# Optimization experiments

Hardware: AMD Instinct MI355X
Metric: run time of the kernel (lower is better)

Reference implementation:

```python
import jax, jax.numpy as jnp
import numpy as np

N, E = 100000, 1600000
NODE_IN, EDGE_IN, H = 128, 16, 128


def sage_conv(x, src, dst, Wl, Wr, b, n_nodes):
    # PyG SAGEConv (aggr='mean'): out = lin_l(mean_{j->i} x_j) + lin_r(x_i), bias on lin_l
    msg_sum = jax.ops.segment_sum(x[src], dst, num_segments=n_nodes)      # [N, d]
    cnt = jax.ops.segment_sum(jnp.ones((src.shape[0],), x.dtype), dst, num_segments=n_nodes)
    mean = msg_sum / jnp.maximum(cnt, 1.0)[:, None]                        # empty neighborhoods -> 0
    return mean @ Wl + x @ Wr + b


def setup_inputs() -> dict:
    key = jax.random.key(0)
    ks = jax.random.split(key, 12)
    s = lambda d: 1.0 / np.sqrt(d)
    return {
        "x": jax.random.normal(ks[0], (N, NODE_IN), jnp.float32),
        "edge_index": jax.random.randint(ks[1], (2, E), 0, N, dtype=jnp.int64),
        "edge_attr": jax.random.normal(ks[2], (E, EDGE_IN), jnp.float32),
        "Wl1": jax.random.normal(ks[3], (NODE_IN, H), jnp.float32) * s(NODE_IN),
        "Wr1": jax.random.normal(ks[4], (NODE_IN, H), jnp.float32) * s(NODE_IN),
        "b1": jnp.zeros((H,), jnp.float32),
        "Wl2": jax.random.normal(ks[5], (H, H), jnp.float32) * s(H),
        "Wr2": jax.random.normal(ks[6], (H, H), jnp.float32) * s(H),
        "b2": jnp.zeros((H,), jnp.float32),
        "Wm1": jax.random.normal(ks[7], (2 * H + EDGE_IN, H), jnp.float32) * s(2 * H + EDGE_IN),
        "bm1": jnp.zeros((H,), jnp.float32),
        "Wm2": jax.random.normal(ks[8], (H, 1), jnp.float32) * s(H),
        "bm2": jnp.zeros((1,), jnp.float32),
    }


def reference(x, edge_index, edge_attr, Wl1, Wr1, b1, Wl2, Wr2, b2, Wm1, bm1, Wm2, bm2):
    src, dst = edge_index[0], edge_index[1]
    h = jax.nn.relu(sage_conv(x, src, dst, Wl1, Wr1, b1, N))
    h = jax.nn.relu(sage_conv(h, src, dst, Wl2, Wr2, b2, N))
    edge_feat = jnp.concatenate([h[src], h[dst], edge_attr], axis=1)  # [E, 2H+edge_in]
    out = jax.nn.relu(edge_feat @ Wm1 + bm1) @ Wm2 + bm2               # dropout is identity in eval
    return out.reshape(-1)
```

## Files before the change

### kernel.cpp

```cpp
#include <hip/hip_runtime.h>

typedef _Float16 f16;
typedef _Float16 f16x2 __attribute__((ext_vector_type(2)));
typedef _Float16 f16x8 __attribute__((ext_vector_type(8)));
typedef float f32x4 __attribute__((ext_vector_type(4)));

#define MFMA16(a,b,c) __builtin_amdgcn_mfma_f32_16x16x32_f16((a),(b),(c),0,0,0)

__global__ void k_detect(const long long* ei, int n_nodes, int* flag) {
    long long v = ei[threadIdx.x];
    int bad = (v < 0 || v >= n_nodes);
    unsigned long long m = __ballot(bad);
    if (threadIdx.x == 0) *flag = (m == 0ULL);
}

__global__ void k_idx(const void* ei, int E, const int* __restrict__ flag,
                      int* __restrict__ src, int* __restrict__ dst,
                      int* __restrict__ deg) {
    int e = blockIdx.x * 256 + threadIdx.x;
    if (e >= E) return;
    int s, d;
    if (*flag) {
        const long long* p = (const long long*)ei;
        s = (int)p[e];
        d = (int)p[(size_t)E + e];
    } else {
        const int* p = (const int*)ei;
        s = p[e];
        d = p[(size_t)E + e];
    }
    src[e] = s;
    dst[e] = d;
    atomicAdd(&deg[d], 1);
}

__device__ __forceinline__ void wfrag_body(const float* Wa, const float* Wb,
                                           f16* dst, int t) {
    int l = t & 63;
    int s = t >> 9;
    int k0 = s * 32 + (l >> 4) * 8;
    int j = ((t >> 6) & 7) * 16 + (l & 15);
    f16x8 h;
    #pragma unroll
    for (int e = 0; e < 8; e++) {
        int k = k0 + e;
        float v = (k < 128) ? Wa[k * 128 + j] : Wb[(k - 128) * 128 + j];
        h[e] = (f16)v;
    }
    *(f16x8*)(dst + (size_t)t * 8) = h;
}

__global__ void k_prep(const float* __restrict__ x,
                       const float* __restrict__ Wl1, const float* __restrict__ Wr1,
                       const float* __restrict__ Wl2, const float* __restrict__ Wr2,
                       const float* __restrict__ Wm1,
                       f16* __restrict__ xh, f16* __restrict__ w1f, f16* __restrict__ w2f,
                       f16* __restrict__ zwf, f16* __restrict__ wef, int N) {
    const int xb = (N * 16 + 255) / 256;
    int b = blockIdx.x;
    if (b < xb) {
        int i = (b * 256 + threadIdx.x) * 8;
        if (i >= N * 128) return;
        float4 a = *(const float4*)(x + i);
        float4 c = *(const float4*)(x + i + 4);
        f16x8 h;
        h[0] = (f16)a.x; h[1] = (f16)a.y; h[2] = (f16)a.z; h[3] = (f16)a.w;
        h[4] = (f16)c.x; h[5] = (f16)c.y; h[6] = (f16)c.z; h[7] = (f16)c.w;
        *(f16x8*)(xh + i) = h;
        return;
    }
    b -= xb;
    if (b < 16) {
        wfrag_body(Wl1, Wr1, w1f, b * 256 + threadIdx.x);
        return;
    }
    if (b < 32) {
        wfrag_body(Wl2, Wr2, w2f, (b - 16) * 256 + threadIdx.x);
        return;
    }
    if (b < 48) {
        int t = (b - 32) * 256 + threadIdx.x;
        int lane = t & 63, c = (t >> 6) & 15, s = t >> 10;
        int k0 = s * 32 + (lane >> 4) * 8;
        int j = c * 16 + (lane & 15);
        f16x8 h;
        #pragma unroll
        for (int e = 0; e < 8; e++) {
            int k = k0 + e;
            float v = (j < 128) ? Wm1[k * 128 + j] : Wm1[(128 + k) * 128 + (j - 128)];
            h[e] = (f16)v;
        }
        *(f16x8*)(zwf + (size_t)t * 8) = h;
        return;
    }
    {
        int t = (b - 48) * 256 + threadIdx.x;
        if (t >= 8 * 64) return;
        int lane = t & 63, ct = t >> 6;
        int k0 = (lane >> 4) * 8;
        int j = (ct >> 1) * 32 + 2 * (lane & 15) + (ct & 1);
        f16x8 h;
        #pragma unroll
        for (int e = 0; e < 8; e++) {
            int k = k0 + e;
            h[e] = (k < 16) ? (f16)Wm1[(256 + k) * 128 + j] : (f16)0.0f;
        }
        *(f16x8*)(wef + (size_t)t * 8) = h;
    }
}

__global__ void k_bsum(const int* __restrict__ deg, int n, int* __restrict__ bsum) {
    __shared__ int ws[4];
    const int tid = threadIdx.x;
    int i = blockIdx.x * 1024 + tid * 4;
    int s = 0;
    if (i + 3 < n) {
        int4 d = *(const int4*)(deg + i);
        s = d.x + d.y + d.z + d.w;
    } else {
        #pragma unroll
        for (int j = 0; j < 4; j++) if (i + j < n) s += deg[i + j];
    }
    #pragma unroll
    for (int m = 1; m < 64; m <<= 1) s += __shfl_xor(s, m, 64);
    if ((tid & 63) == 0) ws[tid >> 6] = s;
    __syncthreads();
    if (tid == 0) bsum[blockIdx.x] = ws[0] + ws[1] + ws[2] + ws[3];
}

__global__ void k_bscan(int* __restrict__ bsum, int nb, int* __restrict__ rowptr_n) {
    __shared__ int wsum[4];
    const int tid = threadIdx.x, lane = tid & 63, wid = tid >> 6;
    int v = (tid < nb) ? bsum[tid] : 0;
    int inc = v;
    #pragma unroll
    for (int off = 1; off < 64; off <<= 1) {
        int u = __shfl_up(inc, off, 64);
        if (lane >= off) inc += u;
    }
    if (lane == 63) wsum[wid] = inc;
    __syncthreads();
    int woff = 0;
    for (int j = 0; j < wid; j++) woff += wsum[j];
    int excl = woff + inc - v;
    if (tid < nb) bsum[tid] = excl;
    if (tid == nb - 1) rowptr_n[0] = excl + v;
}

__global__ void k_rowptr(const int* __restrict__ deg, int n, const int* __restrict__ boff,
                         int* __restrict__ rowptr, int* __restrict__ cursor) {
    __shared__ int wsum[4];
    const int tid = threadIdx.x, lane = tid & 63, wid = tid >> 6;
    int i = blockIdx.x * 1024 + tid * 4;
    int d0 = 0, d1 = 0, d2 = 0, d3 = 0;
    if (i + 3 < n) {
        int4 d = *(const int4*)(deg + i);
        d0 = d.x; d1 = d.y; d2 = d.z; d3 = d.w;
    } else {
        if (i     < n) d0 = deg[i];
        if (i + 1 < n) d1 = deg[i + 1];
        if (i + 2 < n) d2 = deg[i + 2];
        if (i + 3 < n) d3 = deg[i + 3];
    }
    int s = d0 + d1 + d2 + d3;
    int inc = s;
    #pragma unroll
    for (int off = 1; off < 64; off <<= 1) {
        int u = __shfl_up(inc, off, 64);
        if (lane >= off) inc += u;
    }
    if (lane == 63) wsum[wid] = inc;
    __syncthreads();
    int woff = 0;
    for (int j = 0; j < wid; j++) woff += wsum[j];
    int excl = boff[blockIdx.x] + woff + inc - s;
    int e1 = excl + d0, e2 = e1 + d1, e3 = e2 + d2;
    if (i     < n) { rowptr[i]     = excl; cursor[i]     = excl; }
    if (i + 1 < n) { rowptr[i + 1] = e1;   cursor[i + 1] = e1; }
    if (i + 2 < n) { rowptr[i + 2] = e2;   cursor[i + 2] = e2; }
    if (i + 3 < n) { rowptr[i + 3] = e3;   cursor[i + 3] = e3; }
}

__global__ void k_scatter(const int* __restrict__ src, const int* __restrict__ dst, int E,
                          int* __restrict__ cursor, int* __restrict__ col,
                          int4* __restrict__ pk) {
    int e = blockIdx.x * 256 + threadIdx.x;
    if (e < E) {
        int s = src[e], d = dst[e];
        int p = atomicAdd(&cursor[d], 1);
        col[p] = s;
        pk[p] = make_int4(s, e, d, 0);
    }
}

#define AP 136
template<int DO_Z>
__global__ __launch_bounds__(256, DO_Z ? 4 : 5) void k_fuse(
    const f16* __restrict__ tab,
    const int* __restrict__ rowptr, const int* __restrict__ col,
    const f16* __restrict__ Wf, const float* __restrict__ bias,
    const f16* __restrict__ zwf, const float* __restrict__ bm1,
    f16* __restrict__ out, int n_rows) {
    __shared__ __align__(16) f16 sA[64 * AP];
    const int tid = threadIdx.x, lane = tid & 63, w = tid >> 6;
    const int l15 = lane & 15, g = lane >> 4;
    const int base = blockIdx.x * 64;

    const int g16 = tid >> 4, c = tid & 15;
    #pragma unroll
    for (int rep = 0; rep < 4; rep++) {
        const int node = base + rep * 16 + g16;
        float acc[8] = {0.f, 0.f, 0.f, 0.f, 0.f, 0.f, 0.f, 0.f};
        int d = 1;
        if (node < n_rows) {
            const int s0 = rowptr[node], s1 = rowptr[node + 1];
            int k = s0;
            for (; k + 3 < s1; k += 4) {
                const int n0 = col[k], n1 = col[k + 1], n2 = col[k + 2], n3 = col[k + 3];
                f16x8 v0 = *(const f16x8*)(tab + (size_t)n0 * 128 + c * 8);
                f16x8 v1 = *(const f16x8*)(tab + (size_t)n1 * 128 + c * 8);
                f16x8 v2 = *(const f16x8*)(tab + (size_t)n2 * 128 + c * 8);
                f16x8 v3 = *(const f16x8*)(tab + (size_t)n3 * 128 + c * 8);
                #pragma unroll
                for (int j = 0; j < 8; j++)
                    acc[j] += ((float)v0[j] + (float)v1[j]) + ((float)v2[j] + (float)v3[j]);
            }
            for (; k < s1; ++k) {
                const int n0 = col[k];
                f16x8 v0 = *(const f16x8*)(tab + (size_t)n0 * 128 + c * 8);
                #pragma unroll
                for (int j = 0; j < 8; j++) acc[j] += (float)v0[j];
            }
            d = s1 - s0; if (d < 1) d = 1;
        }
        const float inv = 1.f / (float)d;
        f16x8 r;
        #pragma unroll
        for (int j = 0; j < 8; j++) r[j] = (f16)(acc[j] * inv);
        *(f16x8*)&sA[(rep * 16 + g16) * AP + c * 8] = r;
    }
    __syncthreads();

    const int c0 = (2 * w) * 16 + l15, c1 = c0 + 16;
    const float b0 = bias[c0], b1 = bias[c1];
    f32x4 acc[4][2];
    #pragma unroll
    for (int t = 0; t < 4; t++) {
        acc[t][0] = f32x4{b0, b0, b0, b0};
        acc[t][1] = f32x4{b1, b1, b1, b1};
    }
    #pragma unroll
    for (int s = 0; s < 8; s++) {
        f16x8 bf0 = *(const f16x8*)&Wf[((size_t)(s * 8 + 2 * w    ) * 64 + lane) * 8];
        f16x8 bf1 = *(const f16x8*)&Wf[((size_t)(s * 8 + 2 * w + 1) * 64 + lane) * 8];
        const int koff = (s & 3) * 32 + g * 8;
        #pragma unroll
        for (int t = 0; t < 4; t++) {
            f16x8 a;
            if (s < 4) {
                a = *(const f16x8*)&sA[(t * 16 + l15) * AP + koff];
            } else {
                int row = base + t * 16 + l15;
                if (row >= n_rows) row = n_rows - 1;
                a = *(const f16x8*)(tab + (size_t)row * 128 + koff);
            }
            acc[t][0] = MFMA16(a, bf0, acc[t][0]);
            acc[t][1] = MFMA16(a, bf1, acc[t][1]);
        }
    }

    if (DO_Z == 0) {
        #pragma unroll
        for (int t = 0; t < 4; t++) {
            #pragma unroll
            for (int i = 0; i < 4; i++) {
                int row = base + t * 16 + g * 4 + i;
                if (row < n_rows) {
                    float v0 = acc[t][0][i]; v0 = v0 > 0.f ? v0 : 0.f;
                    float v1 = acc[t][1][i]; v1 = v1 > 0.f ? v1 : 0.f;
                    out[(size_t)row * 128 + c0] = (f16)v0;
                    out[(size_t)row * 128 + c1] = (f16)v1;
                }
            }
        }
    } else {
        __syncthreads();
        #pragma unroll
        for (int t = 0; t < 4; t++) {
            #pragma unroll
            for (int i = 0; i < 4; i++) {
                const int rl = t * 16 + g * 4 + i;
                float v0 = acc[t][0][i]; v0 = v0 > 0.f ? v0 : 0.f;
                float v1 = acc[t][1][i]; v1 = v1 > 0.f ? v1 : 0.f;
                sA[rl * AP + c0] = (f16)v0;
                sA[rl * AP + c1] = (f16)v1;
            }
        }
        __syncthreads();
        #pragma unroll
        for (int half = 0; half < 2; half++) {
            const int j0 = (4 * w + 2 * half) * 16 + l15, j1 = j0 + 16;
            const float zb0 = (j0 >= 128) ? bm1[j0 - 128] : 0.0f;
            const float zb1 = (j1 >= 128) ? bm1[j1 - 128] : 0.0f;
            f32x4 zacc[4][2];
            #pragma unroll
            for (int t = 0; t < 4; t++) {
                zacc[t][0] = f32x4{zb0, zb0, zb0, zb0};
                zacc[t][1] = f32x4{zb1, zb1, zb1, zb1};
            }
            #pragma unroll
            for (int s = 0; s < 4; s++) {
                f16x8 wf0 = *(const f16x8*)&zwf[((size_t)(s * 16 + 4 * w + 2 * half    ) * 64 + lane) * 8];
                f16x8 wf1 = *(const f16x8*)&zwf[((size_t)(s * 16 + 4 * w + 2 * half + 1) * 64 + lane) * 8];
                const int koff = s * 32 + g * 8;
                #pragma unroll
                for (int t = 0; t < 4; t++) {
                    f16x8 a = *(const f16x8*)&sA[(t * 16 + l15) * AP + koff];
                    zacc[t][0] = MFMA16(a, wf0, zacc[t][0]);
                    zacc[t][1] = MFMA16(a, wf1, zacc[t][1]);
                }
            }
            #pragma unroll
            for (int t = 0; t < 4; t++) {
                #pragma unroll
                for (int i = 0; i < 4; i++) {
                    int row = base + t * 16 + g * 4 + i;
                    if (row < n_rows) {
                        out[(size_t)row * 256 + j0] = (f16)zacc[t][0][i];
                        out[(size_t)row * 256 + j1] = (f16)zacc[t][1][i];
                    }
                }
            }
        }
    }
}

#define ZP3 136
__global__ __launch_bounds__(256, 4) void k_edge3(
    const f16* __restrict__ z, const float* __restrict__ ea,
    const int4* __restrict__ pk,
    const f16* __restrict__ wef, const float* __restrict__ Wm2,
    const float* __restrict__ bm2, float* __restrict__ out,
    int E, int iters, int nwaves) {
    __shared__ __align__(16) f16 sZ[4][16 * ZP3];
    const int tid = threadIdx.x, lane = tid & 63, w = tid >> 6;
    const int l15 = lane & 15, g = lane >> 4;
    const int te = lane >> 2, sq = lane & 3;
    const int gw = blockIdx.x * 4 + w;

    f16x8 be[8];
    #pragma unroll
    for (int cc = 0; cc < 8; cc++)
        be[cc] = *(const f16x8*)(wef + ((size_t)(cc * 64 + lane)) * 8);
    float2 w2p[4];
    #pragma unroll
    for (int pg = 0; pg < 4; pg++)
        w2p[pg] = *(const float2*)&Wm2[pg * 32 + 2 * l15];
    const float bv = bm2[0];

    f16* myZ = &sZ[w][0];

    f16x8 zs[4], zd[4];
    f16x8 a_cur, a_next;
    int eid_cur, eid_next;

    auto stage_load = [&](int pbase, f16x8* zsv, f16x8* zdv, f16x8& av, int& eidv) {
        int pr = pbase + te; if (pr > E - 1) pr = E - 1;
        const int4 v = pk[pr];
        const int is = v.x, ee = v.y, id = v.z;
        eidv = ee;
        const f16* ps = z + (size_t)is * 256 + sq * 8;
        const f16* pd = z + (size_t)id * 256 + 128 + sq * 8;
        #pragma unroll
        for (int i = 0; i < 4; i++) {
            zsv[i] = *(const f16x8*)(ps + i * 32);
            zdv[i] = *(const f16x8*)(pd + i * 32);
        }
        int pe = pbase + l15; if (pe > E - 1) pe = E - 1;
        f16x8 av_ = {};
        if (g < 2) {
            const int ee2 = pk[pe].y;
            float4 e0 = *(const float4*)(ea + (size_t)ee2 * 16 + g * 8);
            float4 e1 = *(const float4*)(ea + (size_t)ee2 * 16 + g * 8 + 4);
            av_[0] = (f16)e0.x; av_[1] = (f16)e0.y; av_[2] = (f16)e0.z; av_[3] = (f16)e0.w;
            av_[4] = (f16)e1.x; av_[5] = (f16)e1.y; av_[6] = (f16)e1.z; av_[7] = (f16)e1.w;
        }
        av = av_;
    };
    auto stage_write = [&]() {
        f16* zp = myZ + te * ZP3 + sq * 8;
        #pragma unroll
        for (int i = 0; i < 4; i++) {
            f16x8 v = zs[i] + zd[i];
            *(f16x8*)(zp + i * 32) = v;
        }
    };

    stage_load(gw * 16, zs, zd, a_cur, eid_cur);
    stage_write();

    for (int it = 0; it < iters; ++it) {
        const int pbase = (gw + it * nwaves) * 16;
        if (pbase >= E) break;
        const int nxt = (gw + (it + 1) * nwaves) * 16;
        const bool has_next = (it + 1 < iters) && (nxt < E);
        if (has_next) stage_load(nxt, zs, zd, a_next, eid_next);

        f32x4 acc[8];
        #pragma unroll
        for (int cc = 0; cc < 8; cc++) acc[cc] = f32x4{0.f, 0.f, 0.f, 0.f};
        #pragma unroll
        for (int cc = 0; cc < 8; cc++) acc[cc] = MFMA16(a_cur, be[cc], acc[cc]);

        float p[4];
        #pragma unroll
        for (int i = 0; i < 4; i++) {
            const int edge = g * 4 + i;
            float s = 0.f;
            #pragma unroll
            for (int pg = 0; pg < 4; pg++) {
                f16x2 zz = *(const f16x2*)&myZ[edge * ZP3 + pg * 32 + 2 * l15];
                float v0 = (float)zz[0] + acc[2 * pg    ][i]; v0 = v0 > 0.f ? v0 : 0.f;
                float v1 = (float)zz[1] + acc[2 * pg + 1][i]; v1 = v1 > 0.f ? v1 : 0.f;
                s += v0 * w2p[pg].x + v1 * w2p[pg].y;
            }
            p[i] = s;
        }
        #pragma unroll
        for (int m = 1; m < 16; m <<= 1)
            #pragma unroll
            for (int i = 0; i < 4; i++) p[i] += __shfl_xor(p[i], m, 64);
        #pragma unroll
        for (int i = 0; i < 4; i++) {
            int esrc = (lane & 48) + 4 * i;
            int ei_ = __shfl(eid_cur, esrc, 64);
            if (l15 == 0) {
                int pp = pbase + g * 4 + i;
                if (pp < E) out[ei_] = p[i] + bv;
            }
        }
        if (has_next) {
            stage_write();
            a_cur = a_next;
            eid_cur = eid_next;
        }
    }
}

extern "C" void kernel_launch(void* const* d_in, const int* in_sizes, int n_in,
                              void* d_out, int out_size, void* d_ws, size_t ws_size,
                              hipStream_t stream) {
    const float* x   = (const float*)d_in[0];
    const void*  ei  = d_in[1];
    const float* ea  = (const float*)d_in[2];
    const float* Wl1 = (const float*)d_in[3];
    const float* Wr1 = (const float*)d_in[4];
    const float* b1  = (const float*)d_in[5];
    const float* Wl2 = (const float*)d_in[6];
    const float* Wr2 = (const float*)d_in[7];
    const float* b2  = (const float*)d_in[8];
    const float* Wm1 = (const float*)d_in[9];
    const float* bm1 = (const float*)d_in[10];
    const float* Wm2 = (const float*)d_in[11];
    const float* bm2 = (const float*)d_in[12];

    const int N = in_sizes[0] / 128;
    const int E = in_sizes[1] / 2;

    char* ws = (char*)d_ws;
    size_t off = 0;
    auto alloc = [&](size_t bytes) -> void* {
        void* p = ws + off;
        off = (off + bytes + 255) & ~(size_t)255;
        return p;
    };
    f16* z      = (f16*)alloc((size_t)N * 256 * 2);
    f16* xh     = z;
    f16* h1     = (f16*)alloc((size_t)N * 128 * 2);
    int* src    = (int*)alloc((size_t)E * 4);
    int* dst    = (int*)alloc((size_t)E * 4);
    int* col    = (int*)alloc((size_t)E * 4);
    int4* pk    = (int4*)alloc((size_t)E * 16);
    int* deg    = (int*)alloc((size_t)N * 4);
    int* rowptr = (int*)alloc((size_t)(N + 1) * 4);
    int* cursor = (int*)alloc((size_t)N * 4);
    int* bsum   = (int*)alloc((size_t)1024 * 4);
    f16* w1f    = (f16*)alloc((size_t)8 * 8 * 64 * 8 * 2);
    f16* w2f    = (f16*)alloc((size_t)8 * 8 * 64 * 8 * 2);
    f16* zwf    = (f16*)alloc((size_t)4 * 16 * 64 * 8 * 2);
    f16* wef    = (f16*)alloc((size_t)8 * 64 * 8 * 2);
    int* flag   = (int*)alloc(4);
    if (off > ws_size) return;

    const int eb = (E + 255) / 256;
    const int nbk = (N + 1023) / 1024;
    const int rb64 = (N + 63) / 64;

    k_detect<<<1, 64, 0, stream>>>((const long long*)ei, N, flag);
    hipMemsetAsync(deg, 0, (size_t)N * 4, stream);
    k_idx<<<eb, 256, 0, stream>>>(ei, E, flag, src, dst, deg);
    const int xb = (N * 16 + 255) / 256;
    k_prep<<<xb + 50, 256, 0, stream>>>(x, Wl1, Wr1, Wl2, Wr2, Wm1,
                                        xh, w1f, w2f, zwf, wef, N);

    k_bsum<<<nbk, 256, 0, stream>>>(deg, N, bsum);
    k_bscan<<<1, 256, 0, stream>>>(bsum, nbk, rowptr + N);
    k_rowptr<<<nbk, 256, 0, stream>>>(deg, N, bsum, rowptr, cursor);
    k_scatter<<<eb, 256, 0, stream>>>(src, dst, E, cursor, col, pk);

    k_fuse<0><<<rb64, 256, 0, stream>>>(xh, rowptr, col, w1f, b1, nullptr, nullptr, h1, N);
    k_fuse<1><<<rb64, 256, 0, stream>>>(h1, rowptr, col, w2f, b2, zwf, bm1, z, N);

    const int eg = 2048;
    const int nwaves = eg * 4;
    const int ntiles = (E + 15) / 16;
    const int e_iters = (ntiles + nwaves - 1) / nwaves;
    k_edge3<<<eg, 256, 0, stream>>>(z, ea, pk, wef, Wm2, bm2,
                                    (float*)d_out, E, e_iters, nwaves);
}
```

Before: 530.1 us.

## Write edge outputs in CSR order and permute back with a gather kernel

Measured after the change: 502.8 us. 1.05x faster.

```diff
diff --git a/kernel.cpp b/kernel.cpp
--- a/kernel.cpp
+++ b/kernel.cpp
@@ -70,14 +70,8 @@
         return;
     }
     b -= xb;
-    if (b < 16) {
-        wfrag_body(Wl1, Wr1, w1f, b * 256 + threadIdx.x);
-        return;
-    }
-    if (b < 32) {
-        wfrag_body(Wl2, Wr2, w2f, (b - 16) * 256 + threadIdx.x);
-        return;
-    }
+    if (b < 16) { wfrag_body(Wl1, Wr1, w1f, b * 256 + threadIdx.x); return; }
+    if (b < 32) { wfrag_body(Wl2, Wr2, w2f, (b - 16) * 256 + threadIdx.x); return; }
     if (b < 48) {
         int t = (b - 32) * 256 + threadIdx.x;
         int lane = t & 63, c = (t >> 6) & 15, s = t >> 10;
@@ -183,13 +177,14 @@
 
 __global__ void k_scatter(const int* __restrict__ src, const int* __restrict__ dst, int E,
                           int* __restrict__ cursor, int* __restrict__ col,
-                          int4* __restrict__ pk) {
+                          int4* __restrict__ pk, int* __restrict__ pos) {
     int e = blockIdx.x * 256 + threadIdx.x;
     if (e < E) {
         int s = src[e], d = dst[e];
         int p = atomicAdd(&cursor[d], 1);
         col[p] = s;
         pk[p] = make_int4(s, e, d, 0);
+        pos[e] = p;
     }
 }
 
@@ -340,7 +335,7 @@
     const f16* __restrict__ z, const float* __restrict__ ea,
     const int4* __restrict__ pk,
     const f16* __restrict__ wef, const float* __restrict__ Wm2,
-    const float* __restrict__ bm2, float* __restrict__ out,
+    const float* __restrict__ bm2, float* __restrict__ tmp,
     int E, int iters, int nwaves) {
     __shared__ __align__(16) f16 sZ[4][16 * ZP3];
     const int tid = threadIdx.x, lane = tid & 63, w = tid >> 6;
@@ -362,13 +357,11 @@
 
     f16x8 zs[4], zd[4];
     f16x8 a_cur, a_next;
-    int eid_cur, eid_next;
-
-    auto stage_load = [&](int pbase, f16x8* zsv, f16x8* zdv, f16x8& av, int& eidv) {
+
+    auto stage_load = [&](int pbase, f16x8* zsv, f16x8* zdv, f16x8& av) {
         int pr = pbase + te; if (pr > E - 1) pr = E - 1;
         const int4 v = pk[pr];
-        const int is = v.x, ee = v.y, id = v.z;
-        eidv = ee;
+        const int is = v.x, id = v.z;
         const f16* ps = z + (size_t)is * 256 + sq * 8;
         const f16* pd = z + (size_t)id * 256 + 128 + sq * 8;
         #pragma unroll
@@ -396,7 +389,7 @@
         }
     };
 
-    stage_load(gw * 16, zs, zd, a_cur, eid_cur);
+    stage_load(gw * 16, zs, zd, a_cur);
     stage_write();
 
     for (int it = 0; it < iters; ++it) {
@@ -404,7 +397,7 @@
         if (pbase >= E) break;
         const int nxt = (gw + (it + 1) * nwaves) * 16;
         const bool has_next = (it + 1 < iters) && (nxt < E);
-        if (has_next) stage_load(nxt, zs, zd, a_next, eid_next);
+        if (has_next) stage_load(nxt, zs, zd, a_next);
 
         f32x4 acc[8];
         #pragma unroll
@@ -430,21 +423,24 @@
         for (int m = 1; m < 16; m <<= 1)
             #pragma unroll
             for (int i = 0; i < 4; i++) p[i] += __shfl_xor(p[i], m, 64);
-        #pragma unroll
-        for (int i = 0; i < 4; i++) {
-            int esrc = (lane & 48) + 4 * i;
-            int ei_ = __shfl(eid_cur, esrc, 64);
-            if (l15 == 0) {
+        if (l15 == 0) {
+            #pragma unroll
+            for (int i = 0; i < 4; i++) {
                 int pp = pbase + g * 4 + i;
-                if (pp < E) out[ei_] = p[i] + bv;
+                if (pp < E) tmp[pp] = p[i] + bv;
             }
         }
         if (has_next) {
             stage_write();
             a_cur = a_next;
-            eid_cur = eid_next;
-        }
-    }
+        }
+    }
+}
+
+__global__ void k_perm(const float* __restrict__ tmp, const int* __restrict__ pos,
+                       float* __restrict__ out, int E) {
+    int e = blockIdx.x * 256 + threadIdx.x;
+    if (e < E) out[e] = tmp[pos[e]];
 }
 
 extern "C" void kernel_launch(void* const* d_in, const int* in_sizes, int n_in,
@@ -481,6 +477,8 @@
     int* dst    = (int*)alloc((size_t)E * 4);
     int* col    = (int*)alloc((size_t)E * 4);
     int4* pk    = (int4*)alloc((size_t)E * 16);
+    int* pos    = (int*)alloc((size_t)E * 4);
+    float* tmp  = (float*)alloc((size_t)E * 4);
     int* deg    = (int*)alloc((size_t)N * 4);
     int* rowptr = (int*)alloc((size_t)(N + 1) * 4);
     int* cursor = (int*)alloc((size_t)N * 4);
@@ -506,15 +504,16 @@
     k_bsum<<<nbk, 256, 0, stream>>>(deg, N, bsum);
     k_bscan<<<1, 256, 0, stream>>>(bsum, nbk, rowptr + N);
     k_rowptr<<<nbk, 256, 0, stream>>>(deg, N, bsum, rowptr, cursor);
-    k_scatter<<<eb, 256, 0, stream>>>(src, dst, E, cursor, col, pk);
+    k_scatter<<<eb, 256, 0, stream>>>(src, dst, E, cursor, col, pk, pos);
 
     k_fuse<0><<<rb64, 256, 0, stream>>>(xh, rowptr, col, w1f, b1, nullptr, nullptr, h1, N);
     k_fuse<1><<<rb64, 256, 0, stream>>>(h1, rowptr, col, w2f, b2, zwf, bm1, z, N);
 
-    const int eg = 2048;
+    const int eg = 1792;
     const int nwaves = eg * 4;
     const int ntiles = (E + 15) / 16;
     const int e_iters = (ntiles + nwaves - 1) / nwaves;
     k_edge3<<<eg, 256, 0, stream>>>(z, ea, pk, wef, Wm2, bm2,
-                                    (float*)d_out, E, e_iters, nwaves);
-}
+                                    tmp, E, e_iters, nwaves);
+    k_perm<<<eb, 256, 0, stream>>>(tmp, pos, (float*)d_out, E);
+}
```
